# Kernel optimization log

Hardware: AMD Instinct MI355X
Metric: run time of the kernel (lower is better)

The kernel has to match this reference:

```python
import jax, jax.numpy as jnp
import numpy as np

N = 50000      # nodes
E = 800000     # edges (before self-loops)
F_IN = 128
H = 4          # heads
C = 64         # per-head channels
G = 64         # graphs in batch
NEG_SLOPE = 0.2


def setup_inputs() -> dict:
    key = jax.random.key(0)
    ks = jax.random.split(key, 20)
    rn = lambda k, shape, s=0.1: (jax.random.normal(k, shape, jnp.float32) * s)
    x = jax.random.normal(ks[0], (N, F_IN), jnp.float32)
    edge_index = jax.random.randint(ks[1], (2, E), 0, N, dtype=jnp.int32)
    batch = jnp.sort(jax.random.randint(ks[2], (N,), 0, G, dtype=jnp.int32))
    return {
        "x": x, "edge_index": edge_index, "batch": batch,
        # layer 0: 128 -> (4 heads x 64), concat
        "W0": rn(ks[3], (F_IN, H * C)), "a_src0": rn(ks[4], (H, C)), "a_dst0": rn(ks[5], (H, C)), "b0": jnp.zeros((H * C,), jnp.float32),
        "W1": rn(ks[6], (H * C, H * C)), "a_src1": rn(ks[7], (H, C)), "a_dst1": rn(ks[8], (H, C)), "b1": jnp.zeros((H * C,), jnp.float32),
        "W2": rn(ks[9], (H * C, C)), "a_src2": rn(ks[10], (1, C)), "a_dst2": rn(ks[11], (1, C)), "b2": jnp.zeros((C,), jnp.float32),
        "lin_w": rn(ks[12], (C, 1)), "lin_b": jnp.zeros((1,), jnp.float32),
    }


def gat_layer(h_in, src, dst, W, a_src, a_dst, b, heads, ch, concat):
    n = h_in.shape[0]
    h = (h_in @ W).reshape(n, heads, ch)                         # [N,H,C]
    e_src = jnp.sum(h * a_src[None], axis=-1)                    # [N,H]
    e_dst = jnp.sum(h * a_dst[None], axis=-1)                    # [N,H]
    e = jax.nn.leaky_relu(e_src[src] + e_dst[dst], NEG_SLOPE)    # [E,H]
    # segment softmax over incoming edges of each destination node
    m = jax.ops.segment_max(e, dst, num_segments=n)
    m = jnp.where(jnp.isneginf(m), 0.0, m)
    ex = jnp.exp(e - m[dst])
    denom = jax.ops.segment_sum(ex, dst, num_segments=n)
    alpha = ex / (denom[dst] + 1e-16)                            # [E,H]
    out = jax.ops.segment_sum(h[src] * alpha[:, :, None], dst, num_segments=n)  # [N,H,C]
    out = out.reshape(n, heads * ch) if concat else out.mean(axis=1)
    return out + b


def reference(x, edge_index, batch, W0, a_src0, a_dst0, b0, W1, a_src1, a_dst1, b1, W2, a_src2, a_dst2, b2, lin_w, lin_b):
    n = x.shape[0]
    loops = jnp.arange(n, dtype=edge_index.dtype)
    src = jnp.concatenate([edge_index[0], loops])  # PyG add_self_loops=True
    dst = jnp.concatenate([edge_index[1], loops])
    h = jax.nn.relu(gat_layer(x, src, dst, W0, a_src0, a_dst0, b0, H, C, True))
    h = jax.nn.relu(gat_layer(h, src, dst, W1, a_src1, a_dst1, b1, H, C, True))
    h = gat_layer(h, src, dst, W2, a_src2, a_dst2, b2, 1, C, False)  # [N,64]
    # global mean pool per graph
    counts = jax.ops.segment_sum(jnp.ones((n,), h.dtype), batch, num_segments=G)
    pooled = jax.ops.segment_sum(h, batch, num_segments=G) / jnp.maximum(counts, 1.0)[:, None]
    return pooled @ lin_w + lin_b  # [G,1]
```

## Files before the change

kernel.cpp:

```cpp
#include <hip/hip_runtime.h>
#include <math.h>

typedef __bf16 bf16x8 __attribute__((ext_vector_type(8)));
typedef __bf16 bf16x4 __attribute__((ext_vector_type(4)));
typedef float f32x4 __attribute__((ext_vector_type(4)));
typedef float f32x2 __attribute__((ext_vector_type(2)));
typedef unsigned int u32x2 __attribute__((ext_vector_type(2)));
typedef unsigned int u32x4 __attribute__((ext_vector_type(4)));

#define LOG2E 1.4426950408889634f
#define BCAP 8192

static __device__ __forceinline__ float lrelu(float e) { return e > 0.0f ? e : 0.2f * e; }
static __device__ __forceinline__ float fexp2(float x) { return __builtin_amdgcn_exp2f(x); }

static __device__ __forceinline__ void dec16(u32x4 u, float* f) {
#pragma unroll
  for (int i = 0; i < 4; i++) {
    f32x2 a = __builtin_amdgcn_cvt_pk_f32_fp8(u[i], false);
    f32x2 b = __builtin_amdgcn_cvt_pk_f32_fp8(u[i], true);
    f[i * 4 + 0] = a.x;
    f[i * 4 + 1] = a.y;
    f[i * 4 + 2] = b.x;
    f[i * 4 + 3] = b.y;
  }
}

static __device__ __forceinline__ void dec8(unsigned int lo, unsigned int hi, float* f) {
  f32x2 a = __builtin_amdgcn_cvt_pk_f32_fp8(lo, false);
  f32x2 b = __builtin_amdgcn_cvt_pk_f32_fp8(lo, true);
  f32x2 c = __builtin_amdgcn_cvt_pk_f32_fp8(hi, false);
  f32x2 d = __builtin_amdgcn_cvt_pk_f32_fp8(hi, true);
  f[0] = a.x; f[1] = a.y; f[2] = b.x; f[3] = b.y;
  f[4] = c.x; f[5] = c.y; f[6] = d.x; f[7] = d.y;
}

static __device__ __forceinline__ int cmap(int p) {
  return (p & ~63) + (p & 3) * 16 + ((p & 63) >> 2);
}

__global__ void prep_kernel(const float* __restrict__ x, __bf16* __restrict__ xb, int n4,
                            const float* __restrict__ W0, __bf16* __restrict__ Bt0,
                            const float* __restrict__ W1, __bf16* __restrict__ Bt1,
                            const float* __restrict__ W2, __bf16* __restrict__ Bt2, int FIN,
                            int* __restrict__ cnt, int n) {
  int cb = (n4 + 255) / 256;
  int b = blockIdx.x;
  if (b < cb) {
    int i = b * 256 + threadIdx.x;
    if (i < n4) {
      f32x4 v = ((const f32x4*)x)[i];
      bf16x4 o = {(__bf16)v.x, (__bf16)v.y, (__bf16)v.z, (__bf16)v.w};
      ((bf16x4*)xb)[i] = o;
    }
    return;
  }
  b -= cb;
  if (b < 256) {
    for (int k = threadIdx.x; k < FIN; k += 256) Bt0[b * FIN + k] = (__bf16)W0[k * 256 + b];
    return;
  }
  b -= 256;
  if (b < 256) {
    int k = threadIdx.x;
    Bt1[b * 256 + k] = (__bf16)W1[cmap(k) * 256 + b];
    return;
  }
  b -= 256;
  if (b < 64) {
    int k = threadIdx.x;
    Bt2[b * 256 + k] = (__bf16)W2[cmap(k) * 64 + b];
    return;
  }
  b -= 64;
  int i = b * 256 + threadIdx.x;
  if (i < n) cnt[i] = 0;
}

template <int K, int NT>
__global__ __launch_bounds__(256) void gemm_part_kernel(
    const __bf16* __restrict__ A, const __bf16* __restrict__ Bt,
    const float* __restrict__ a_src, const float* __restrict__ a_dst,
    unsigned char* __restrict__ C, float* __restrict__ es, float* __restrict__ ed, int M,
    int gmx, const int* __restrict__ srcE, const int* __restrict__ dstE,
    int* __restrict__ bucket_cnt, unsigned int* __restrict__ part, int E, int EE, int n) {
  constexpr int Nc = NT * 64;
  constexpr int H = NT;
  __shared__ __bf16 Bs[NT * 64][40];
  if ((int)blockIdx.x >= gmx) {
    int tid = threadIdx.x;
    int* hist = (int*)&Bs[0][0];
    int* gbase = hist + 256;
    hist[tid] = 0;
    __syncthreads();
    int ab = ((int)blockIdx.x - gmx) * 4096;
    int sv[16], dv[16];
#pragma unroll
    for (int t = 0; t < 16; t++) {
      int e = ab + t * 256 + tid;
      if (e < EE) {
        if (e < E) { sv[t] = srcE[e]; dv[t] = dstE[e]; }
        else { sv[t] = dv[t] = e - E; }
      } else { sv[t] = -1; dv[t] = 0; }
    }
    int lr[16];
#pragma unroll
    for (int t = 0; t < 16; t++)
      if (sv[t] >= 0) lr[t] = atomicAdd(&hist[dv[t] >> 8], 1);
    __syncthreads();
    int NB = (n + 255) >> 8;
    gbase[tid] = (tid < NB && hist[tid] > 0) ? atomicAdd(&bucket_cnt[tid * 16], hist[tid]) : 0;
    __syncthreads();
#pragma unroll
    for (int t = 0; t < 16; t++)
      if (sv[t] >= 0) {
        int bk = dv[t] >> 8;
        part[(size_t)bk * BCAP + gbase[bk] + lr[t]] =
            (unsigned int)sv[t] | ((unsigned int)(dv[t] & 255) << 24);
      }
    return;
  }
  int bid = blockIdx.x;
  int tid = threadIdx.x;
  int wave = tid >> 6;
  int lane = tid & 63;
  int quad = lane >> 4;
  int l16 = lane & 15;
  int rowBase = bid * 64 + wave * 16;
  f32x4 acc[NT * 4] = {};
  int arow = rowBase + l16;
  arow = (arow < M) ? arow : (M - 1);
  const __bf16* Aptr = &A[(size_t)arow * K + quad * 8];
  int sr = tid >> 2;
  int sc = (tid & 3) * 8;
  for (int kb = 0; kb < K; kb += 32) {
#pragma unroll
    for (int it = 0; it < NT; it++) {
      int r = it * 64 + sr;
      *(bf16x8*)&Bs[r][sc] = *(const bf16x8*)&Bt[(size_t)r * K + kb + sc];
    }
    __syncthreads();
    bf16x8 a = *(const bf16x8*)&Aptr[kb];
#pragma unroll
    for (int ng = 0; ng < NT * 4; ng++) {
      bf16x8 b = *(const bf16x8*)&Bs[ng * 16 + l16][quad * 8];
      acc[ng] = __builtin_amdgcn_mfma_f32_16x16x32_bf16(a, b, acc[ng], 0, 0, 0);
    }
    __syncthreads();
  }
  float asv[NT * 4], adv[NT * 4];
#pragma unroll
  for (int ng = 0; ng < NT * 4; ng++) {
    int c = (ng >> 2) * 64 + (ng & 3) * 16 + l16;
    asv[ng] = a_src[c];
    adv[ng] = a_dst[c];
  }
#pragma unroll
  for (int r = 0; r < 4; r++) {
    int row = rowBase + quad * 4 + r;
#pragma unroll
    for (int h = 0; h < H; h++) {
      float ss = 0.f, sd = 0.f;
#pragma unroll
      for (int g = 0; g < 4; g++) {
        float hv = acc[h * 4 + g][r];
        ss += hv * asv[h * 4 + g];
        sd += hv * adv[h * 4 + g];
      }
#pragma unroll
      for (int o = 1; o < 16; o <<= 1) {
        ss += __shfl_xor(ss, o);
        sd += __shfl_xor(sd, o);
      }
      if (row < M) {
        if (l16 == 0) {
          es[row * H + h] = ss * LOG2E;
          ed[row * H + h] = sd * LOG2E;
        }
        unsigned int pk = 0;
        pk = __builtin_amdgcn_cvt_pk_fp8_f32(acc[h * 4 + 0][r], acc[h * 4 + 1][r], pk, false);
        pk = __builtin_amdgcn_cvt_pk_fp8_f32(acc[h * 4 + 2][r], acc[h * 4 + 3][r], pk, true);
        *(unsigned int*)&C[(size_t)row * Nc + h * 64 + l16 * 4] = pk;
      }
    }
  }
}

__global__ __launch_bounds__(1024) void bucket_csr_kernel(
    const unsigned int* __restrict__ part, const int* __restrict__ bucket_cnt,
    int* __restrict__ offsets, int* __restrict__ src_sorted, int n, int EE) {
  __shared__ int sc[256];
  __shared__ int excl[256];
  __shared__ int run[256];
  int tid = threadIdx.x;
  int b = blockIdx.x;
  int NB = (n + 255) >> 8;
  if (tid < 256) sc[tid] = (tid < NB) ? bucket_cnt[tid * 16] : 0;
  __syncthreads();
  for (int d = 1; d < 256; d <<= 1) {
    int t = 0;
    if (tid < 256 && tid >= d) t = sc[tid - d];
    __syncthreads();
    if (tid < 256) sc[tid] += t;
    __syncthreads();
  }
  int base = (b == 0) ? 0 : sc[b - 1];
  int cb = sc[b] - base;
  const unsigned int* mypart = part + (size_t)b * BCAP;
  if (tid < 256) run[tid] = 0;
  __syncthreads();
  for (int i = tid; i < cb; i += 1024) atomicAdd(&run[mypart[i] >> 24], 1);
  __syncthreads();
  int myc = (tid < 256) ? run[tid] : 0;
  if (tid < 256) sc[tid] = myc;
  __syncthreads();
  for (int d = 1; d < 256; d <<= 1) {
    int t = 0;
    if (tid < 256 && tid >= d) t = sc[tid - d];
    __syncthreads();
    if (tid < 256) sc[tid] += t;
    __syncthreads();
  }
  if (tid < 256) {
    excl[tid] = sc[tid] - myc;
    int node = b * 256 + tid;
    if (node < n) offsets[node] = base + excl[tid];
    run[tid] = 0;
  }
  if (b == 0 && tid == 0) offsets[n] = EE;
  __syncthreads();
  for (int i = tid; i < cb; i += 1024) {
    unsigned int p = mypart[i];
    int j = p >> 24;
    int r = atomicAdd(&run[j], 1);
    src_sorted[base + excl[j] + r] = (int)(p & 0xFFFFFFu);
  }
}

template <int K, int NT>
__global__ __launch_bounds__(256) void gemm2_kernel(const __bf16* __restrict__ A,
                                                    const __bf16* __restrict__ Bt,
                                                    const float* __restrict__ a_src,
                                                    const float* __restrict__ a_dst,
                                                    unsigned char* __restrict__ C,
                                                    float* __restrict__ es,
                                                    float* __restrict__ ed, int M) {
  constexpr int Nc = NT * 64;
  constexpr int H = NT;
  __shared__ __bf16 Bs[NT * 64][40];
  int tid = threadIdx.x;
  int wave = tid >> 6;
  int lane = tid & 63;
  int quad = lane >> 4;
  int l16 = lane & 15;
  int rowBase = blockIdx.x * 64 + wave * 16;
  f32x4 acc[NT * 4] = {};
  int arow = rowBase + l16;
  arow = (arow < M) ? arow : (M - 1);
  const __bf16* Aptr = &A[(size_t)arow * K + quad * 8];
  int sr = tid >> 2;
  int sc = (tid & 3) * 8;
  for (int kb = 0; kb < K; kb += 32) {
#pragma unroll
    for (int it = 0; it < NT; it++) {
      int r = it * 64 + sr;
      *(bf16x8*)&Bs[r][sc] = *(const bf16x8*)&Bt[(size_t)r * K + kb + sc];
    }
    __syncthreads();
    bf16x8 a = *(const bf16x8*)&Aptr[kb];
#pragma unroll
    for (int ng = 0; ng < NT * 4; ng++) {
      bf16x8 b = *(const bf16x8*)&Bs[ng * 16 + l16][quad * 8];
      acc[ng] = __builtin_amdgcn_mfma_f32_16x16x32_bf16(a, b, acc[ng], 0, 0, 0);
    }
    __syncthreads();
  }
  float asv[NT * 4], adv[NT * 4];
#pragma unroll
  for (int ng = 0; ng < NT * 4; ng++) {
    int c = (ng >> 2) * 64 + (ng & 3) * 16 + l16;
    asv[ng] = a_src[c];
    adv[ng] = a_dst[c];
  }
#pragma unroll
  for (int r = 0; r < 4; r++) {
    int row = rowBase + quad * 4 + r;
#pragma unroll
    for (int h = 0; h < H; h++) {
      float ss = 0.f, sd = 0.f;
#pragma unroll
      for (int g = 0; g < 4; g++) {
        float hv = acc[h * 4 + g][r];
        ss += hv * asv[h * 4 + g];
        sd += hv * adv[h * 4 + g];
      }
#pragma unroll
      for (int o = 1; o < 16; o <<= 1) {
        ss += __shfl_xor(ss, o);
        sd += __shfl_xor(sd, o);
      }
      if (row < M) {
        if (l16 == 0) {
          es[row * H + h] = ss * LOG2E;
          ed[row * H + h] = sd * LOG2E;
        }
        unsigned int pk = 0;
        pk = __builtin_amdgcn_cvt_pk_fp8_f32(acc[h * 4 + 0][r], acc[h * 4 + 1][r], pk, false);
        pk = __builtin_amdgcn_cvt_pk_fp8_f32(acc[h * 4 + 2][r], acc[h * 4 + 3][r], pk, true);
        *(unsigned int*)&C[(size_t)row * Nc + h * 64 + l16 * 4] = pk;
      }
    }
  }
}

__global__ void agg256_kernel(const unsigned char* __restrict__ h, const int* __restrict__ offsets,
                              const int* __restrict__ src_sorted, const float* __restrict__ es,
                              const float* __restrict__ ed, const float* __restrict__ bias,
                              __bf16* __restrict__ out, int n) {
  int node = blockIdx.x * (blockDim.x >> 6) + (threadIdx.x >> 6);
  int lane = threadIdx.x & 63;
  if (node >= n) return;
  int quad = lane >> 4;
  int l16 = lane & 15;
  int hd = l16 >> 2;
  float myEd = ed[node * 4 + hd];
  int off = offsets[node];
  int deg = offsets[node + 1] - off;
  float acc[16] = {};
  float sw = 0.f;
  int j = 0;
  int s0a = 0, s1a = 0;
  if (j + 8 <= deg) {
    s0a = src_sorted[off + j + quad];
    s1a = src_sorted[off + j + 4 + quad];
  }
  for (; j + 8 <= deg;) {
    int jn = j + 8;
    int s0 = s0a, s1 = s1a;
    if (jn + 8 <= deg) {
      s0a = src_sorted[off + jn + quad];
      s1a = src_sorted[off + jn + 4 + quad];
    }
    float e0 = es[s0 * 4 + hd];
    float e1 = es[s1 * 4 + hd];
    u32x4 u0 = *(const u32x4*)&h[(size_t)s0 * 256 + l16 * 16];
    u32x4 u1 = *(const u32x4*)&h[(size_t)s1 * 256 + l16 * 16];
    float w0 = fexp2(lrelu(e0 + myEd));
    float w1 = fexp2(lrelu(e1 + myEd));
    sw += w0 + w1;
    float f[16];
    dec16(u0, f);
#pragma unroll
    for (int k = 0; k < 16; k++) acc[k] += w0 * f[k];
    dec16(u1, f);
#pragma unroll
    for (int k = 0; k < 16; k++) acc[k] += w1 * f[k];
    j = jn;
  }
  for (; j < deg; j += 4) {
    if (quad < deg - j) {
      int s = src_sorted[off + j + quad];
      float w = fexp2(lrelu(es[s * 4 + hd] + myEd));
      sw += w;
      u32x4 u = *(const u32x4*)&h[(size_t)s * 256 + l16 * 16];
      float f[16];
      dec16(u, f);
#pragma unroll
      for (int k = 0; k < 16; k++) acc[k] += w * f[k];
    }
  }
  sw += __shfl_xor(sw, 16);
  sw += __shfl_xor(sw, 32);
#pragma unroll
  for (int k = 0; k < 16; k++) {
    acc[k] += __shfl_xor(acc[k], 16);
    acc[k] += __shfl_xor(acc[k], 32);
  }
  float invS = 1.0f / (sw + 1e-16f);
  if (quad == 0) {
    bf16x8 o0, o1;
#pragma unroll
    for (int k = 0; k < 16; k++) {
      int c = hd * 64 + (k & 3) * 16 + (l16 & 3) * 4 + (k >> 2);
      float v = fmaxf(acc[k] * invS + bias[c], 0.f);
      if (k < 8) o0[k] = (__bf16)v; else o1[k - 8] = (__bf16)v;
    }
    *(bf16x8*)&out[(size_t)node * 256 + l16 * 16] = o0;
    *(bf16x8*)&out[(size_t)node * 256 + l16 * 16 + 8] = o1;
  }
}

__global__ void agg64_kernel(const unsigned char* __restrict__ h, const int* __restrict__ offsets,
                             const int* __restrict__ src_sorted, const float* __restrict__ es,
                             const float* __restrict__ ed, const float* __restrict__ bias,
                             const float* __restrict__ lin_w, float* __restrict__ pnode, int n) {
  int node = blockIdx.x * (blockDim.x >> 6) + (threadIdx.x >> 6);
  int lane = threadIdx.x & 63;
  if (node >= n) return;
  int grp = lane >> 3;
  int l8 = lane & 7;
  float myEd = ed[node];
  int off = offsets[node];
  int deg = offsets[node + 1] - off;
  float acc[8] = {};
  float sw = 0.f;
  int j = 0;
  for (; j + 8 <= deg; j += 8) {
    int s = src_sorted[off + j + grp];
    float w = fexp2(lrelu(es[s] + myEd));
    sw += w;
    u32x2 u = *(const u32x2*)&h[(size_t)s * 64 + l8 * 8];
    float f[8];
    dec8(u.x, u.y, f);
#pragma unroll
    for (int k = 0; k < 8; k++) acc[k] += w * f[k];
  }
  if (j < deg && grp < deg - j) {
    int s = src_sorted[off + j + grp];
    float w = fexp2(lrelu(es[s] + myEd));
    sw += w;
    u32x2 u = *(const u32x2*)&h[(size_t)s * 64 + l8 * 8];
    float f[8];
    dec8(u.x, u.y, f);
#pragma unroll
    for (int k = 0; k < 8; k++) acc[k] += w * f[k];
  }
#pragma unroll
  for (int o = 8; o < 64; o <<= 1) {
    sw += __shfl_xor(sw, o);
#pragma unroll
    for (int k = 0; k < 8; k++) acc[k] += __shfl_xor(acc[k], o);
  }
  float invS = 1.0f / (sw + 1e-16f);
  float p = 0.f;
#pragma unroll
  for (int k = 0; k < 8; k++) {
    int c = (k & 3) * 16 + l8 * 2 + (k >> 2);
    p += (acc[k] * invS + bias[c]) * lin_w[c];
  }
#pragma unroll
  for (int o = 1; o < 8; o <<= 1) p += __shfl_xor(p, o);
  if (lane == 0) pnode[node] = p;
}

static __device__ __forceinline__ int lowerb(const int* __restrict__ a, int n, int key) {
  int lo = 0, hi = n;
  while (lo < hi) {
    int mid = (lo + hi) >> 1;
    if (a[mid] < key) lo = mid + 1; else hi = mid;
  }
  return lo;
}

__global__ void poolfinal_kernel(const float* __restrict__ pnode, const int* __restrict__ batch,
                                 const float* __restrict__ lin_b, float* __restrict__ out, int n) {
  __shared__ float ws[4];
  int g = blockIdx.x;
  int start = lowerb(batch, n, g);
  int end = lowerb(batch, n, g + 1);
  float acc = 0.f;
  for (int i = start + threadIdx.x; i < end; i += 256) acc += pnode[i];
  for (int o = 32; o > 0; o >>= 1) acc += __shfl_down(acc, o);
  if ((threadIdx.x & 63) == 0) ws[threadIdx.x >> 6] = acc;
  __syncthreads();
  if (threadIdx.x == 0) {
    float total = ws[0] + ws[1] + ws[2] + ws[3];
    out[g] = total / fmaxf((float)(end - start), 1.0f) + lin_b[0];
  }
}

extern "C" void kernel_launch(void* const* d_in, const int* in_sizes, int n_in, void* d_out,
                              int out_size, void* d_ws, size_t ws_size, hipStream_t stream) {
  const float* x = (const float*)d_in[0];
  const int* edge_index = (const int*)d_in[1];
  const int* batch = (const int*)d_in[2];
  const float* W0 = (const float*)d_in[3];
  const float* a_src0 = (const float*)d_in[4];
  const float* a_dst0 = (const float*)d_in[5];
  const float* b0 = (const float*)d_in[6];
  const float* W1 = (const float*)d_in[7];
  const float* a_src1 = (const float*)d_in[8];
  const float* a_dst1 = (const float*)d_in[9];
  const float* b1 = (const float*)d_in[10];
  const float* W2 = (const float*)d_in[11];
  const float* a_src2 = (const float*)d_in[12];
  const float* a_dst2 = (const float*)d_in[13];
  const float* b2 = (const float*)d_in[14];
  const float* lin_w = (const float*)d_in[15];
  const float* lin_b = (const float*)d_in[16];
  float* out = (float*)d_out;

  const int N = in_sizes[2];
  const int E = in_sizes[1] / 2;
  const int EE = E + N;
  const int G = 64;
  const int FIN = in_sizes[0] / N;

  const int* srcArr = edge_index;
  const int* dstArr = edge_index + E;

  size_t off = 0;
  auto alloc = [&](size_t bytes) -> void* {
    off = (off + 255) & ~(size_t)255;
    void* p = (char*)d_ws + off;
    off += bytes;
    return p;
  };
  __bf16* xb = (__bf16*)alloc((size_t)N * FIN * 2);
  unsigned char* hA = (unsigned char*)alloc((size_t)N * 256);
  __bf16* hB = (__bf16*)alloc((size_t)N * 256 * 2);
  unsigned char* h2 = (unsigned char*)alloc((size_t)N * 64);
  float* pnode = (float*)alloc((size_t)N * 4);
  __bf16* Bt0 = (__bf16*)alloc((size_t)256 * FIN * 2);
  __bf16* Bt1 = (__bf16*)alloc((size_t)256 * 256 * 2);
  __bf16* Bt2 = (__bf16*)alloc((size_t)64 * 256 * 2);
  float* es = (float*)alloc((size_t)N * 4 * 4);
  float* ed = (float*)alloc((size_t)N * 4 * 4);
  int* offsets = (int*)alloc((size_t)(N + 1) * 4);
  int* src_sorted = (int*)alloc((size_t)EE * 4);
  int* bucket_cnt = (int*)alloc((size_t)4096 * 4);
  (void)ws_size;

  int NB = (N + 255) >> 8;

  unsigned int* part = (unsigned int*)hB;

  int n4 = N * FIN / 4;
  int cb = (n4 + 255) / 256;
  int nwb = (N + 3) / 4;
  int gmx = (N + 63) / 64;
  int nA = (EE + 4095) / 4096;

  prep_kernel<<<cb + 576 + 16, 256, 0, stream>>>(x, xb, n4, W0, Bt0, W1, Bt1, W2, Bt2, FIN,
                                                 bucket_cnt, 4096);

  gemm_part_kernel<128, 4><<<gmx + nA, 256, 0, stream>>>(
      xb, Bt0, a_src0, a_dst0, hA, es, ed, N, gmx, srcArr, dstArr, bucket_cnt, part, E, EE, N);

  bucket_csr_kernel<<<NB, 1024, 0, stream>>>(part, bucket_cnt, offsets, src_sorted, N, EE);

  agg256_kernel<<<nwb, 256, 0, stream>>>(hA, offsets, src_sorted, es, ed, b0, hB, N);

  gemm2_kernel<256, 4><<<gmx, 256, 0, stream>>>(hB, Bt1, a_src1, a_dst1, hA, es, ed, N);
  agg256_kernel<<<nwb, 256, 0, stream>>>(hA, offsets, src_sorted, es, ed, b1, hB, N);

  gemm2_kernel<256, 1><<<gmx, 256, 0, stream>>>(hB, Bt2, a_src2, a_dst2, h2, es, ed, N);
  agg64_kernel<<<nwb, 256, 0, stream>>>(h2, offsets, src_sorted, es, ed, b2, lin_w, pnode, N);

  poolfinal_kernel<<<G, 256, 0, stream>>>(pnode, batch, lin_b, out, N);
}
```

Measured before the change: 288.4 us.

## Double-buffer B tile in LDS and preload all A fragments in GEMM kernels

Both GEMM kernels now load every A fragment for the full K range into registers up front. They also keep two LDS buffers for the B tile, so the next K-slice is written while MFMAs run on the current one, and only one barrier is needed per step. The aim is to hide global-load latency behind compute and remove a barrier per K iteration. In exchange, register pressure grows with K/32 A fragments and the shared memory footprint doubles, which may lower occupancy. The edge-partition branch now addresses its histogram through the 3-D buffer.

```diff
diff --git a/kernel.cpp b/kernel.cpp
--- a/kernel.cpp
+++ b/kernel.cpp
@@ -86,10 +86,11 @@
     int* __restrict__ bucket_cnt, unsigned int* __restrict__ part, int E, int EE, int n) {
   constexpr int Nc = NT * 64;
   constexpr int H = NT;
-  __shared__ __bf16 Bs[NT * 64][40];
+  constexpr int KS = K / 32;
+  __shared__ __bf16 Bs[2][NT * 64][40];
   if ((int)blockIdx.x >= gmx) {
     int tid = threadIdx.x;
-    int* hist = (int*)&Bs[0][0];
+    int* hist = (int*)&Bs[0][0][0];
     int* gbase = hist + 256;
     hist[tid] = 0;
     __syncthreads();
@@ -133,18 +134,29 @@
   const __bf16* Aptr = &A[(size_t)arow * K + quad * 8];
   int sr = tid >> 2;
   int sc = (tid & 3) * 8;
-  for (int kb = 0; kb < K; kb += 32) {
-#pragma unroll
-    for (int it = 0; it < NT; it++) {
-      int r = it * 64 + sr;
-      *(bf16x8*)&Bs[r][sc] = *(const bf16x8*)&Bt[(size_t)r * K + kb + sc];
-    }
-    __syncthreads();
-    bf16x8 a = *(const bf16x8*)&Aptr[kb];
+  bf16x8 af[KS];
+#pragma unroll
+  for (int s = 0; s < KS; s++) af[s] = *(const bf16x8*)&Aptr[s * 32];
+#pragma unroll
+  for (int it = 0; it < NT; it++) {
+    int r = it * 64 + sr;
+    *(bf16x8*)&Bs[0][r][sc] = *(const bf16x8*)&Bt[(size_t)r * K + sc];
+  }
+  __syncthreads();
+#pragma unroll
+  for (int s = 0; s < KS; s++) {
+    int cur = s & 1;
+    if (s + 1 < KS) {
+#pragma unroll
+      for (int it = 0; it < NT; it++) {
+        int r = it * 64 + sr;
+        *(bf16x8*)&Bs[cur ^ 1][r][sc] = *(const bf16x8*)&Bt[(size_t)r * K + (s + 1) * 32 + sc];
+      }
+    }
 #pragma unroll
     for (int ng = 0; ng < NT * 4; ng++) {
-      bf16x8 b = *(const bf16x8*)&Bs[ng * 16 + l16][quad * 8];
-      acc[ng] = __builtin_amdgcn_mfma_f32_16x16x32_bf16(a, b, acc[ng], 0, 0, 0);
+      bf16x8 b = *(const bf16x8*)&Bs[cur][ng * 16 + l16][quad * 8];
+      acc[ng] = __builtin_amdgcn_mfma_f32_16x16x32_bf16(af[s], b, acc[ng], 0, 0, 0);
     }
     __syncthreads();
   }
@@ -247,7 +259,8 @@
                                                     float* __restrict__ ed, int M) {
   constexpr int Nc = NT * 64;
   constexpr int H = NT;
-  __shared__ __bf16 Bs[NT * 64][40];
+  constexpr int KS = K / 32;
+  __shared__ __bf16 Bs[2][NT * 64][40];
   int tid = threadIdx.x;
   int wave = tid >> 6;
   int lane = tid & 63;
@@ -260,18 +273,29 @@
   const __bf16* Aptr = &A[(size_t)arow * K + quad * 8];
   int sr = tid >> 2;
   int sc = (tid & 3) * 8;
-  for (int kb = 0; kb < K; kb += 32) {
-#pragma unroll
-    for (int it = 0; it < NT; it++) {
-      int r = it * 64 + sr;
-      *(bf16x8*)&Bs[r][sc] = *(const bf16x8*)&Bt[(size_t)r * K + kb + sc];
-    }
-    __syncthreads();
-    bf16x8 a = *(const bf16x8*)&Aptr[kb];
+  bf16x8 af[KS];
+#pragma unroll
+  for (int s = 0; s < KS; s++) af[s] = *(const bf16x8*)&Aptr[s * 32];
+#pragma unroll
+  for (int it = 0; it < NT; it++) {
+    int r = it * 64 + sr;
+    *(bf16x8*)&Bs[0][r][sc] = *(const bf16x8*)&Bt[(size_t)r * K + sc];
+  }
+  __syncthreads();
+#pragma unroll
+  for (int s = 0; s < KS; s++) {
+    int cur = s & 1;
+    if (s + 1 < KS) {
+#pragma unroll
+      for (int it = 0; it < NT; it++) {
+        int r = it * 64 + sr;
+        *(bf16x8*)&Bs[cur ^ 1][r][sc] = *(const bf16x8*)&Bt[(size_t)r * K + (s + 1) * 32 + sc];
+      }
+    }
 #pragma unroll
     for (int ng = 0; ng < NT * 4; ng++) {
-      bf16x8 b = *(const bf16x8*)&Bs[ng * 16 + l16][quad * 8];
-      acc[ng] = __builtin_amdgcn_mfma_f32_16x16x32_bf16(a, b, acc[ng], 0, 0, 0);
+      bf16x8 b = *(const bf16x8*)&Bs[cur][ng * 16 + l16][quad * 8];
+      acc[ng] = __builtin_amdgcn_mfma_f32_16x16x32_bf16(af[s], b, acc[ng], 0, 0, 0);
     }
     __syncthreads();
   }
```

Result: no change. 286.1 us (-0.8%).
